# Performance work log

Measured on AMD Instinct MI355X. Metric: run time of the kernel, lower is better.

## Reference

```python
import jax, jax.numpy as jnp
import numpy as np

N_NODES = 80000
N_EDGES = 160000
HID = 300
NODE_DIM = 133
EDGE_DIM = 14
N_GRAPHS = 1600


def setup_inputs() -> dict:
    key = jax.random.key(0)
    ks = jax.random.split(key, 32)
    s = 0.05
    half = N_EDGES // 2
    inp = {
        "x": jax.random.normal(ks[0], (N_NODES, NODE_DIM), jnp.float32),
        "edge_attr": jax.random.normal(ks[1], (N_EDGES, EDGE_DIM), jnp.float32),
        "W_atoms": jax.random.uniform(ks[2], (N_NODES,), jnp.float32),
        "eps": jax.random.normal(ks[3], (N_GRAPHS, HID), jnp.float32),
        "src_half": jax.random.randint(ks[4], (half,), 0, N_NODES, jnp.int32),
        "dst_half": jax.random.randint(ks[5], (half,), 0, N_NODES, jnp.int32),
        "batch": jnp.sort(jax.random.randint(ks[6], (N_NODES,), 0, N_GRAPHS, jnp.int32)),
    }
    def W(k, i, o):
        return jax.random.normal(k, (i, o), jnp.float32) * s
    def B(k, o):
        return jax.random.normal(k, (o,), jnp.float32) * s
    # tconv1 (first_linear=True): lin1 in=node+edge, atom_updater in=node+hid (with ReLU)
    inp["t_lin_w"] = W(ks[7], NODE_DIM + EDGE_DIM, HID); inp["t_lin_b"] = B(ks[8], HID)
    inp["t_mp_w"] = jax.random.normal(ks[9], (3, HID, HID), jnp.float32) * s
    inp["t_mp_b"] = jax.random.normal(ks[10], (3, HID), jnp.float32) * s
    inp["t_au_w"] = W(ks[11], NODE_DIM + HID, HID); inp["t_au_b"] = B(ks[12], HID)
    # mu conv (first_linear=False): lin2 in=hid+edge, atom_updater2 in=2*hid (no ReLU)
    inp["mu_lin_w"] = W(ks[13], HID + EDGE_DIM, HID); inp["mu_lin_b"] = B(ks[14], HID)
    inp["mu_mp_w"] = jax.random.normal(ks[15], (3, HID, HID), jnp.float32) * s
    inp["mu_mp_b"] = jax.random.normal(ks[16], (3, HID), jnp.float32) * s
    inp["mu_au_w"] = W(ks[17], 2 * HID, HID); inp["mu_au_b"] = B(ks[18], HID)
    # logvar conv (first_linear=False)
    inp["lv_lin_w"] = W(ks[19], HID + EDGE_DIM, HID); inp["lv_lin_b"] = B(ks[20], HID)
    inp["lv_mp_w"] = jax.random.normal(ks[21], (3, HID, HID), jnp.float32) * s
    inp["lv_mp_b"] = jax.random.normal(ks[22], (3, HID), jnp.float32) * s
    inp["lv_au_w"] = W(ks[23], 2 * HID, HID); inp["lv_au_b"] = B(ks[24], HID)
    return inp


def reference(x, edge_attr, W_atoms, eps, src_half, dst_half, batch,
              t_lin_w, t_lin_b, t_mp_w, t_mp_b, t_au_w, t_au_b,
              mu_lin_w, mu_lin_b, mu_mp_w, mu_mp_b, mu_au_w, mu_au_b,
              lv_lin_w, lv_lin_b, lv_mp_w, lv_mp_b, lv_au_w, lv_au_b):
    E = edge_attr.shape[0]
    half = E // 2
    N = x.shape[0]
    # directed edges come in reverse pairs: edge e and edge rev(e)
    src = jnp.concatenate([src_half, dst_half])
    dst = jnp.concatenate([dst_half, src_half])
    rev = jnp.concatenate([jnp.arange(half, E), jnp.arange(0, half)])
    relu = jax.nn.relu

    def mp_agg(h):
        # dest_is_origin sparse mm: for edge e=(u->v), sum h over edges k with
        # dst(k)==u, excluding the reverse edge (v->u)
        inc = jax.ops.segment_sum(h, dst, num_segments=N)  # [N, H]
        return inc[src] - h[rev]

    def conv(node_in, lin_w, lin_b, mp_w, mp_b, au_w, au_b, out_relu):
        h = relu(jnp.concatenate([node_in[src], edge_attr], axis=1) @ lin_w + lin_b)
        for i in range(3):  # three vec_scratch_MP_layers: relu(h + Lin(D @ h))
            h = relu(h + mp_agg(h) @ mp_w[i] + mp_b[i])
        # inc_edges_to_atom sparse mm: sum incident edge states per atom
        sum_inc = jax.ops.segment_sum(h, dst, num_segments=N)
        a = jnp.concatenate([node_in, sum_inc], axis=1) @ au_w + au_b
        return relu(a) if out_relu else a

    shared = conv(x, t_lin_w, t_lin_b, t_mp_w, t_mp_b, t_au_w, t_au_b, True)
    mu = conv(shared, mu_lin_w, mu_lin_b, mu_mp_w, mu_mp_b, mu_au_w, mu_au_b, False)
    lv = conv(shared, lv_lin_w, lv_lin_b, lv_mp_w, lv_mp_b, lv_au_w, lv_au_b, False)

    w = W_atoms[:, None]
    cnt = jnp.maximum(jax.ops.segment_sum(jnp.ones((N,), x.dtype), batch,
                                          num_segments=N_GRAPHS), 1.0)[:, None]
    mu_g = jax.ops.segment_sum(mu * w, batch, num_segments=N_GRAPHS) / cnt
    lv_g = jax.ops.segment_sum(lv * w, batch, num_segments=N_GRAPHS) / cnt
    # VAE reparameterization: z = mu + exp(0.5*logvar) * eps
    z = mu_g + jnp.exp(0.5 * lv_g) * eps
    return z
```

## Files before the change

kernel.cpp:

```cpp
#include <hip/hip_runtime.h>
#include <hip/hip_bf16.h>

#define NN 80000
#define NE 160000
#define HALF 80000
#define HID 300
#define NG 1600
#define SCB 256

typedef __attribute__((ext_vector_type(8))) short bf16x8v;
typedef __attribute__((ext_vector_type(4))) float f32x4v;

__device__ __forceinline__ float bf2f_us(unsigned short u) {
    return __uint_as_float(((unsigned int)u) << 16);
}
__device__ __forceinline__ unsigned short f2bf_us(float f) {
    union { __bf16 b; unsigned short u; } cv;
    cv.b = (__bf16)f;
    return cv.u;
}
__device__ __forceinline__ float ld1(const float* p) { return *p; }
__device__ __forceinline__ float ld1(const unsigned short* p) { return bf2f_us(*p); }
__device__ __forceinline__ void st1(float* p, float v) { *p = v; }
__device__ __forceinline__ void st1(unsigned short* p, float v) { *p = f2bf_us(v); }
__device__ __forceinline__ float4 ld4(const float* p) { return *(const float4*)p; }
__device__ __forceinline__ float4 ld4(const unsigned short* p) {
    ushort4 u = *(const ushort4*)p;
    return make_float4(bf2f_us(u.x), bf2f_us(u.y), bf2f_us(u.z), bf2f_us(u.w));
}
__device__ __forceinline__ void st4(float* p, float4 v) { *(float4*)p = v; }
__device__ __forceinline__ void st4(unsigned short* p, float4 v) {
    ushort4 u; u.x = f2bf_us(v.x); u.y = f2bf_us(v.y); u.z = f2bf_us(v.z); u.w = f2bf_us(v.w);
    *(ushort4*)p = u;
}
__device__ __forceinline__ int clampi(int v, int lo, int hi) {
    return v < lo ? lo : (v > hi ? hi : v);
}

__global__ void k_zerof(float* __restrict__ p, int n) {
    int i = blockIdx.x * 256 + threadIdx.x; if (i < n) p[i] = 0.f;
}
__global__ void k_zeroi(int* __restrict__ p, int n) {
    int i = blockIdx.x * 256 + threadIdx.x; if (i < n) p[i] = 0;
}

__global__ void k_wsplit_conv(const float* __restrict__ Wmp,
                              const float* __restrict__ Wlin, int Klin, int nktlin,
                              const float* __restrict__ Wau, int Kau, int nktau,
                              unsigned short* __restrict__ wh_mp, unsigned short* __restrict__ wl_mp,
                              unsigned short* __restrict__ wh_la, unsigned short* __restrict__ wl_la) {
    const int MP_L = 10 * 19 * 512;
    int idx = blockIdx.x * 256 + threadIdx.x;
    int total = 570 + nktlin * 19 + nktau * 19;
    int t = idx >> 6;
    if (t >= total) return;
    int lane = idx & 63;
    const float* W; int Krows, ltile;
    unsigned short *whi, *wlo;
    if (t < 570) {
        int l = t / 190, rem = t - l * 190;
        W = Wmp + l * 90000; Krows = 300; ltile = rem;
        whi = wh_mp + l * MP_L; wlo = wl_mp + l * MP_L;
    } else if (t < 570 + nktlin * 19) {
        ltile = t - 570; W = Wlin; Krows = Klin;
        whi = wh_la; wlo = wl_la;
    } else {
        ltile = t - 570 - nktlin * 19; W = Wau; Krows = Kau;
        size_t off = (size_t)nktlin * 19 * 512;
        whi = wh_la + off; wlo = wl_la + off;
    }
    int kt = ltile / 19, ct = ltile - kt * 19;
    int quad = lane >> 4, cr = lane & 15;
    size_t obase = ((size_t)ltile * 64 + lane) * 8;
    for (int j = 0; j < 8; ++j) {
        int k = kt * 32 + quad * 8 + j;
        int n = ct * 16 + cr;
        float v = (k < Krows && n < 300) ? W[(size_t)k * 300 + n] : 0.f;
        unsigned short hu = f2bf_us(v);
        unsigned short lu = f2bf_us(v - bf2f_us(hu));
        whi[obase + j] = hu;
        wlo[obase + j] = lu;
    }
}

__global__ void k_hist(const int* __restrict__ srcH, const int* __restrict__ dstH, int* __restrict__ deg) {
    int e = blockIdx.x * 256 + threadIdx.x;
    if (e >= NE) return;
    int d = (e < HALF) ? dstH[e] : srcH[e - HALF];
    d = clampi(d, 0, NN - 1);
    atomicAdd(&deg[d], 1);
}
__global__ void k_histg(const int* __restrict__ batch, int* __restrict__ degg) {
    int n = blockIdx.x * 256 + threadIdx.x;
    if (n >= NN) return;
    atomicAdd(&degg[clampi(batch[n], 0, NG - 1)], 1);
}

__global__ __launch_bounds__(256) void k_scan_part(const int* __restrict__ deg, int* __restrict__ part, int n) {
    __shared__ int red[256];
    int b = blockIdx.x, t = threadIdx.x;
    int chunk = (n + SCB - 1) / SCB;
// ... 73 lines not shown
    int lo = clampi(start[n], 0, NE), hi = clampi(start[n + 1], 0, NE);
    float4 a0 = make_float4(0.f, 0.f, 0.f, 0.f);
    float4 a1 = make_float4(0.f, 0.f, 0.f, 0.f);
    int j = lo;
    for (; j + 2 <= hi; j += 2) {
        int e0 = clampi(elist[j], 0, NE - 1);
        int e1 = clampi(elist[j + 1], 0, NE - 1);
        const unsigned short* r0 = &h[(size_t)e0 * 300 + c0];
        const unsigned short* r1 = &h[(size_t)e1 * 300 + c0];
        float4 v0 = ld4(r0);
        float4 w0 = ld4(r1);
        a0.x += v0.x + w0.x; a0.y += v0.y + w0.y; a0.z += v0.z + w0.z; a0.w += v0.w + w0.w;
        if (full) {
            float4 v1 = ld4(r0 + 4);
            float4 w1 = ld4(r1 + 4);
            a1.x += v1.x + w1.x; a1.y += v1.y + w1.y; a1.z += v1.z + w1.z; a1.w += v1.w + w1.w;
        }
    }
    if (j < hi) {
        int e0 = clampi(elist[j], 0, NE - 1);
        const unsigned short* r0 = &h[(size_t)e0 * 300 + c0];
        float4 v0 = ld4(r0);
        a0.x += v0.x; a0.y += v0.y; a0.z += v0.z; a0.w += v0.w;
        if (full) {
            float4 v1 = ld4(r0 + 4);
            a1.x += v1.x; a1.y += v1.y; a1.z += v1.z; a1.w += v1.w;
        }
    }
    st4(&inc[(size_t)n * 300 + c0], a0);
    if (full) st4(&inc[(size_t)n * 300 + c0 + 4], a1);
}


template <int NID, typename TN>
__global__ __launch_bounds__(512, 4) void k_lin_mfma(
        const TN* __restrict__ node_in, const float* __restrict__ ea,
        const int* __restrict__ srcH, const int* __restrict__ dstH,
        const unsigned short* __restrict__ whi, const unsigned short* __restrict__ wlo,
        const float* __restrict__ bias, unsigned short* __restrict__ h) {
    constexpr int K = NID + 14;
    constexpr int KP = (K + 31) & ~31;
    constexpr int NKT = KP / 32;
    constexpr int LDK = (KP + 8 < 312) ? 312 : KP + 8;
    __shared__ unsigned short As[64 * LDK];
    __shared__ int ssrc[64];
    const int tid = threadIdx.x;
    const int lane = tid & 63, wv = tid >> 6;
    const int quad = lane >> 4, cr = lane & 15;
    const int e0 = blockIdx.x * 64;
    if (tid < 64) {
        int e = e0 + tid;
        int s = (e < HALF) ? srcH[e] : dstH[e - HALF];
        ssrc[tid] = clampi(s, 0, NN - 1);
    }
    __syncthreads();
    if constexpr (NID == 300) {
        for (int idx = tid; idx < 64 * 75; idx += 512) {
            int r = idx / 75, q = idx - r * 75;
            *(ushort4*)&As[r * LDK + q * 4] =
                *(const ushort4*)&((const unsigned short*)node_in)[(size_t)ssrc[r] * 300 + q * 4];
        }
        for (int idx = tid; idx < 64 * (KP - 300); idx += 512) {
            int r = idx / (KP - 300), k = idx - r * (KP - 300);
            int kk = 300 + k;
            float v = (kk < K) ? ea[(size_t)(e0 + r) * 14 + (kk - 300)] : 0.f;
            As[r * LDK + kk] = f2bf_us(v);
        }
    } else {
        for (int idx = tid; idx < 64 * KP; idx += 512) {
            int r = idx / KP, k = idx - r * KP;
            float v;
            if (k < NID)    v = ld1(&node_in[(size_t)ssrc[r] * NID + k]);
            else if (k < K) v = ea[(size_t)(e0 + r) * 14 + (k - NID)];
            else            v = 0.f;
            As[r * LDK + k] = f2bf_us(v);
        }
    }
    __syncthreads();
    f32x4v acc[4][3];
    #pragma unroll
    for (int c = 0; c < 3; ++c) {
        int ct = wv + 8 * c;
        float b = 0.f;
        if (ct < 19) { int col = ct * 16 + cr; if (col < 300) b = bias[col]; }
        #pragma unroll
        for (int rt = 0; rt < 4; ++rt) { f32x4v a = {b, b, b, b}; acc[rt][c] = a; }
    }
    bf16x8v pbhi[2][3], pblo[2][3];
    #pragma unroll
    for (int c = 0; c < 3; ++c) {
        int ct = wv + 8 * c;
        if (ct < 19) {
            size_t base = ((size_t)ct * 64 + lane) * 8;
            pbhi[0][c] = *(const bf16x8v*)&whi[base];
            pblo[0][c] = *(const bf16x8v*)&wlo[base];
        }
    }
    #pragma unroll
    for (int kt = 0; kt < NKT; ++kt) {
        const int cur = kt & 1, nxt = cur ^ 1;
        if (kt + 1 < NKT) {
            #pragma unroll
            for (int c = 0; c < 3; ++c) {
                int ct = wv + 8 * c;
                if (ct < 19) {
                    size_t base = ((size_t)((kt + 1) * 19 + ct) * 64 + lane) * 8;
                    pbhi[nxt][c] = *(const bf16x8v*)&whi[base];
                    pblo[nxt][c] = *(const bf16x8v*)&wlo[base];
                }
            }
        }
        #pragma unroll
        for (int rt = 0; rt < 4; ++rt) {
            bf16x8v a = *(const bf16x8v*)&As[(rt * 16 + cr) * LDK + kt * 32 + quad * 8];
            #pragma unroll
            for (int c = 0; c < 3; ++c) {
                int ct = wv + 8 * c;
                if (ct >= 19) break;
                acc[rt][c] = __builtin_amdgcn_mfma_f32_16x16x32_bf16(a, pblo[cur][c], acc[rt][c], 0, 0, 0);
                acc[rt][c] = __builtin_amdgcn_mfma_f32_16x16x32_bf16(a, pbhi[cur][c], acc[rt][c], 0, 0, 0);
            }
        }
    }
    __syncthreads();
    #pragma unroll
    for (int c = 0; c < 3; ++c) {
        int ct = wv + 8 * c;
        if (ct >= 19) break;
        int col = ct * 16 + cr;
        if (col >= 300) continue;
        #pragma unroll
        for (int rt = 0; rt < 4; ++rt)
            #pragma unroll
            for (int r = 0; r < 4; ++r)
                As[(rt * 16 + quad * 4 + r) * LDK + col] = f2bf_us(fmaxf(acc[rt][c][r], 0.f));
    }
    __syncthreads();
    for (int idx = tid; idx < 64 * 75; idx += 512) {
        int r = idx / 75, q = idx - r * 75;
        *(ushort4*)&h[(size_t)(e0 + r) * 300 + q * 4] = *(const ushort4*)&As[r * LDK + q * 4];
    }
}

template <int NID, typename TN, bool RELU>
__global__ __launch_bounds__(512, 4) void k_au_mfma(
        const TN* __restrict__ node_in, const unsigned short* __restrict__ h,
        const int* __restrict__ elist, const int* __restrict__ start,
        const unsigned short* __restrict__ whi, const unsigned short* __restrict__ wlo,
        const float* __restrict__ bias, unsigned short* __restrict__ out_rows) {
    constexpr int K = NID + 300;
    constexpr int KP = (K + 31) & ~31;
    constexpr int NKT = KP / 32;
    constexpr int LDK = KP + 8;
    __shared__ unsigned short As[64 * LDK];
    const int tid = threadIdx.x;
    const int lane = tid & 63, wv = tid >> 6;
    const int quad = lane >> 4, cr = lane & 15;
    const int n0 = blockIdx.x * 64;
    if constexpr (NID == 300) {
        for (int idx = tid; idx < 64 * 75; idx += 512) {
            int r = idx / 75, q = idx - r * 75;
            *(ushort4*)&As[r * LDK + q * 4] =
                *(const ushort4*)&((const unsigned short*)node_in)[(size_t)(n0 + r) * 300 + q * 4];
        }
    } else {
        const float* xb = (const float*)node_in + (size_t)n0 * NID;
        for (int f4 = tid; f4 < (64 * NID) / 4; f4 += 512) {
            float4 v = *(const float4*)&xb[f4 * 4];
            int f = f4 * 4;
            float vv[4] = {v.x, v.y, v.z, v.w};
            #pragma unroll
            for (int i = 0; i < 4; ++i) {
                int fi = f + i;
                int r = fi / NID, k = fi - r * NID;
                As[r * LDK + k] = f2bf_us(vv[i]);
            }
        }
    }
    for (int idx = tid; idx < 64 * 75; idx += 512) {
        int r = idx / 75, q = idx - r * 75;
        int n = n0 + r;
        int lo = clampi(start[n], 0, NE), hi = clampi(start[n + 1], 0, NE);
        float4 acc = make_float4(0.f, 0.f, 0.f, 0.f);
        int j = lo;
        for (; j + 2 <= hi; j += 2) {
            int ei0 = clampi(elist[j], 0, NE - 1);
            int ei1 = clampi(elist[j + 1], 0, NE - 1);
            float4 v0 = ld4(&h[(size_t)ei0 * 300 + q * 4]);
            float4 v1 = ld4(&h[(size_t)ei1 * 300 + q * 4]);
            acc.x += v0.x; acc.y += v0.y; acc.z += v0.z; acc.w += v0.w;
            acc.x += v1.x; acc.y += v1.y; acc.z += v1.z; acc.w += v1.w;
        }
        if (j < hi) {
            int ei0 = clampi(elist[j], 0, NE - 1);
            float4 v0 = ld4(&h[(size_t)ei0 * 300 + q * 4]);
            acc.x += v0.x; acc.y += v0.y; acc.z += v0.z; acc.w += v0.w;
        }
        unsigned short* dst = &As[r * LDK + NID + q * 4];
        dst[0] = f2bf_us(acc.x); dst[1] = f2bf_us(acc.y);
        dst[2] = f2bf_us(acc.z); dst[3] = f2bf_us(acc.w);
    }
    constexpr int PAD = KP - NID - 300;
    for (int idx = tid; idx < 64 * PAD; idx += 512) {
        int r = idx / PAD, k = idx - r * PAD;
        As[r * LDK + NID + 300 + k] = 0;
    }
    __syncthreads();
    f32x4v acc[4][3];
    #pragma unroll
    for (int c = 0; c < 3; ++c) {
        int ct = wv + 8 * c;
        float b = 0.f;
        if (ct < 19) { int col = ct * 16 + cr; if (col < 300) b = bias[col]; }
        #pragma unroll
        for (int rt = 0; rt < 4; ++rt) { f32x4v a = {b, b, b, b}; acc[rt][c] = a; }
    }
    bf16x8v pbhi[2][3], pblo[2][3];
    #pragma unroll
    for (int c = 0; c < 3; ++c) {
        int ct = wv + 8 * c;
        if (ct < 19) {
            size_t base = ((size_t)ct * 64 + lane) * 8;
            pbhi[0][c] = *(const bf16x8v*)&whi[base];
            pblo[0][c] = *(const bf16x8v*)&wlo[base];
        }
    }
    #pragma unroll
    for (int kt = 0; kt < NKT; ++kt) {
        const int cur = kt & 1, nxt = cur ^ 1;
        if (kt + 1 < NKT) {
            #pragma unroll
            for (int c = 0; c < 3; ++c) {
                int ct = wv + 8 * c;
                if (ct < 19) {
                    size_t base = ((size_t)((kt + 1) * 19 + ct) * 64 + lane) * 8;
                    pbhi[nxt][c] = *(const bf16x8v*)&whi[base];
                    pblo[nxt][c] = *(const bf16x8v*)&wlo[base];
                }
            }
        }
        #pragma unroll
        for (int rt = 0; rt < 4; ++rt) {
            bf16x8v a = *(const bf16x8v*)&As[(rt * 16 + cr) * LDK + kt * 32 + quad * 8];
            #pragma unroll
            for (int c = 0; c < 3; ++c) {
                int ct = wv + 8 * c;
                if (ct >= 19) break;
                acc[rt][c] = __builtin_amdgcn_mfma_f32_16x16x32_bf16(a, pblo[cur][c], acc[rt][c], 0, 0, 0);
                acc[rt][c] = __builtin_amdgcn_mfma_f32_16x16x32_bf16(a, pbhi[cur][c], acc[rt][c], 0, 0, 0);
            }
        }
    }
    __syncthreads();
    #pragma unroll
    for (int c = 0; c < 3; ++c) {
        int ct = wv + 8 * c;
        if (ct >= 19) break;
        int col = ct * 16 + cr;
        if (col >= 300) continue;
        #pragma unroll
        for (int rt = 0; rt < 4; ++rt)
            #pragma unroll
            for (int r = 0; r < 4; ++r) {
                float v = acc[rt][c][r];
                As[(rt * 16 + quad * 4 + r) * LDK + col] = f2bf_us(RELU ? fmaxf(v, 0.f) : v);
            }
    }
    __syncthreads();
    for (int idx = tid; idx < 64 * 75; idx += 512) {
        int r = idx / 75, q = idx - r * 75;
        *(ushort4*)&out_rows[(size_t)(n0 + r) * 300 + q * 4] = *(const ushort4*)&As[r * LDK + q * 4];
    }
}

__global__ __launch_bounds__(512, 4) void k_mp_mfma(
        unsigned short* __restrict__ h, const unsigned short* __restrict__ inc,
        const int* __restrict__ srcH, const int* __restrict__ dstH,
        const unsigned short* __restrict__ whi, const unsigned short* __restrict__ wlo,
        const float* __restrict__ bias) {
    constexpr int LDK = 328;
    __shared__ unsigned short Hs[64 * LDK];
    __shared__ int ssrc[64];
    const int tid = threadIdx.x;
    const int lane = tid & 63, wv = tid >> 6;
    const int quad = lane >> 4, cr = lane & 15;
    const int p0 = blockIdx.x * 32;
    if (tid < 64) {
        int r = tid;
        int e = (r < 32) ? (p0 + r) : (p0 + r - 32 + HALF);
        int s = (e < HALF) ? srcH[e] : dstH[e - HALF];
        ssrc[r] = clampi(s, 0, NN - 1);
    }
    __syncthreads();
    for (int idx = tid; idx < 64 * 80; idx += 512) {
        int r = idx / 80, q = idx - r * 80;
        int col = q * 4;
        if (col < 300) {
            int ep = (r < 32) ? (p0 + r + HALF) : (p0 + r - 32);
            float4 hp = ld4(&h[(size_t)ep * 300 + col]);
            float4 iv = ld4(&inc[(size_t)ssrc[r] * 300 + col]);
            st4(&Hs[r * LDK + col],
                make_float4(iv.x - hp.x, iv.y - hp.y, iv.z - hp.z, iv.w - hp.w));
        } else {
            *(ushort4*)&Hs[r * LDK + col] = make_ushort4(0, 0, 0, 0);
        }
    }
    __syncthreads();
    f32x4v acc[4][3];
    #pragma unroll
    for (int c = 0; c < 3; ++c)
        #pragma unroll
        for (int rt = 0; rt < 4; ++rt) {
            f32x4v a = {0.f, 0.f, 0.f, 0.f};
            acc[rt][c] = a;
        }
    bf16x8v pbhi[2][3], pblo[2][3];
    #pragma unroll
    for (int c = 0; c < 3; ++c) {
        int ct = wv + 8 * c;
        if (ct < 19) {
            size_t base = ((size_t)ct * 64 + lane) * 8;
            pbhi[0][c] = *(const bf16x8v*)&whi[base];
            pblo[0][c] = *(const bf16x8v*)&wlo[base];
        }
    }
    #pragma unroll
    for (int kt = 0; kt < 10; ++kt) {
        const int cur = kt & 1, nxt = cur ^ 1;
        if (kt + 1 < 10) {
            #pragma unroll
            for (int c = 0; c < 3; ++c) {
                int ct = wv + 8 * c;
                if (ct < 19) {
                    size_t base = ((size_t)((kt + 1) * 19 + ct) * 64 + lane) * 8;
                    pbhi[nxt][c] = *(const bf16x8v*)&whi[base];
                    pblo[nxt][c] = *(const bf16x8v*)&wlo[base];
                }
            }
        }
        #pragma unroll
        for (int rt = 0; rt < 4; ++rt) {
            bf16x8v a = *(const bf16x8v*)&Hs[(rt * 16 + cr) * LDK + kt * 32 + quad * 8];
            #pragma unroll
            for (int c = 0; c < 3; ++c) {
                int ct = wv + 8 * c;
                if (ct >= 19) break;
                acc[rt][c] = __builtin_amdgcn_mfma_f32_16x16x32_bf16(a, pblo[cur][c], acc[rt][c], 0, 0, 0);
                acc[rt][c] = __builtin_amdgcn_mfma_f32_16x16x32_bf16(a, pbhi[cur][c], acc[rt][c], 0, 0, 0);
            }
        }
    }
    __syncthreads();
    #pragma unroll
    for (int c = 0; c < 3; ++c) {
        int ct = wv + 8 * c;
        if (ct >= 19) break;
        int col = ct * 16 + cr;
        if (col >= 300) continue;
        float bv = bias[col];
        #pragma unroll
        for (int rt = 0; rt < 4; ++rt)
            #pragma unroll
            for (int r = 0; r < 4; ++r) {
                int row = rt * 16 + quad * 4 + r;
                int e = (row < 32) ? (p0 + row) : (p0 + row - 32 + HALF);
                float hv = bf2f_us(h[(size_t)e * 300 + col]);
                Hs[row * LDK + col] = f2bf_us(fmaxf(acc[rt][c][r] + bv + hv, 0.f));
            }
    }
    __syncthreads();
    for (int idx = tid; idx < 64 * 75; idx += 512) {
        int r = idx / 75, q = idx - r * 75;
        int e = (r < 32) ? (p0 + r) : (p0 + r - 32 + HALF);
        *(ushort4*)&h[(size_t)e * 300 + q * 4] = *(const ushort4*)&Hs[r * LDK + q * 4];
    }
}

__global__ __launch_bounds__(320) void k_pool(const unsigned short* __restrict__ rows,
                                              const float* __restrict__ wat,
                                              const int* __restrict__ gs, float* __restrict__ outg) {
    int g = blockIdx.x, c = threadIdx.x;
    if (c >= 300) return;
    int lo = clampi(gs[g], 0, NN), hi = clampi(gs[g + 1], 0, NN);
    float acc = 0.f;
    for (int n = lo; n < hi; ++n)
        acc += bf2f_us(rows[(size_t)n * 300 + c]) * wat[n];
    float cn = fmaxf((float)(hi - lo), 1.f);
    outg[g * 300 + c] = acc / cn;
}
__global__ __launch_bounds__(320) void k_final(const float* __restrict__ mu_g, const float* __restrict__ lv_g,
                                               const float* __restrict__ eps, float* __restrict__ out) {
    int g = blockIdx.x, c = threadIdx.x;
    if (c >= 300) return;
    out[g * 300 + c] = mu_g[g * 300 + c] + expf(0.5f * lv_g[g * 300 + c]) * eps[g * 300 + c];
}

extern "C" void kernel_launch(void* const* d_in, const int* in_sizes, int n_in,
                              void* d_out, int out_size, void* d_ws, size_t ws_size,
                              hipStream_t stream) {
    float* outp = (float*)d_out;

    const size_t NEED = 199500000ull;
    if (ws_size < NEED) {
        k_zerof<<<(out_size + 255) / 256, 256, 0, stream>>>(outp, out_size);
        return;
    }

// ... 1 lines not shown
    const float* ea  = (const float*)d_in[1];
    const float* wat = (const float*)d_in[2];
    const float* eps = (const float*)d_in[3];
    const int* srcH  = (const int*)d_in[4];
    const int* dstH  = (const int*)d_in[5];
    const int* batch = (const int*)d_in[6];
    const float* w_t_lin  = (const float*)d_in[7];
    const float* b_t_lin  = (const float*)d_in[8];
    const float* w_t_mp   = (const float*)d_in[9];
    const float* b_t_mp   = (const float*)d_in[10];
    const float* w_t_au   = (const float*)d_in[11];
    const float* b_t_au   = (const float*)d_in[12];
    const float* w_mu_lin = (const float*)d_in[13];
    const float* b_mu_lin = (const float*)d_in[14];
    const float* w_mu_mp  = (const float*)d_in[15];
    const float* b_mu_mp  = (const float*)d_in[16];
    const float* w_mu_au  = (const float*)d_in[17];
    const float* b_mu_au  = (const float*)d_in[18];
    const float* w_lv_lin = (const float*)d_in[19];
    const float* b_lv_lin = (const float*)d_in[20];
    const float* w_lv_mp  = (const float*)d_in[21];
    const float* b_lv_mp  = (const float*)d_in[22];
    const float* w_lv_au  = (const float*)d_in[23];
    const float* b_lv_au  = (const float*)d_in[24];

    char* p = (char*)d_ws;
    auto alloc = [&](size_t nbytes) { char* q = p; p += (nbytes + 255) & ~(size_t)255; return q; };
    unsigned short* h   = (unsigned short*)alloc((size_t)NE * 300 * 2);
    unsigned short* inc = (unsigned short*)alloc((size_t)NN * 300 * 2);
    unsigned short* sh  = (unsigned short*)alloc((size_t)NN * 300 * 2);
    const size_t MPU = (size_t)3 * 10 * 19 * 512;
    unsigned short* wh_mp = (unsigned short*)alloc(MPU * 2);
    unsigned short* wl_mp = (unsigned short*)alloc(MPU * 2);
    const size_t LAU = (size_t)29 * 19 * 512;
    unsigned short* wh_la = (unsigned short*)alloc(LAU * 2);
    unsigned short* wl_la = (unsigned short*)alloc(LAU * 2);
    float* mu_g = (float*)alloc((size_t)NG * 300 * 4);
    float* lv_g = (float*)alloc((size_t)NG * 300 * 4);
    int* deg    = (int*)alloc(NN * 4);
    int* startA = (int*)alloc((NN + 1) * 4);
    int* elist  = (int*)alloc(NE * 4);
    int* degg   = (int*)alloc(NG * 4);
    int* gs     = (int*)alloc((NG + 1) * 4);
    int* part   = (int*)alloc(SCB * 4);

    k_zeroi<<<(NN + 255) / 256, 256, 0, stream>>>(deg, NN);
    k_hist<<<(NE + 255) / 256, 256, 0, stream>>>(srcH, dstH, deg);
    k_scan_part<<<SCB, 256, 0, stream>>>(deg, part, NN);
    k_scan_offsets<<<1, 256, 0, stream>>>(part);
    k_scan_apply<<<SCB, 256, 0, stream>>>(deg, part, startA, deg, NN);
    k_fill<<<(NE + 255) / 256, 256, 0, stream>>>(srcH, dstH, deg, elist);
    k_zeroi<<<(NG + 255) / 256, 256, 0, stream>>>(degg, NG);
    k_histg<<<(NN + 255) / 256, 256, 0, stream>>>(batch, degg);
    k_scan_part<<<SCB, 256, 0, stream>>>(degg, part, NG);
    k_scan_offsets<<<1, 256, 0, stream>>>(part);
    k_scan_apply<<<SCB, 256, 0, stream>>>(degg, part, gs, (int*)nullptr, NG);

    const int SSG = (NN * 38 + 255) / 256;
    const size_t MP_L = (size_t)10 * 19 * 512;
    unsigned short* rows = inc;
    auto wsplit_conv = [&](const float* Wmp, const float* Wlin, int Klin, int nktlin,
                           const float* Wau, int Kau, int nktau) {
        int total = 570 + nktlin * 19 + nktau * 19;
        k_wsplit_conv<<<(total * 64 + 255) / 256, 256, 0, stream>>>(
            Wmp, Wlin, Klin, nktlin, Wau, Kau, nktau, wh_mp, wl_mp, wh_la, wl_la);
    };

    wsplit_conv(w_t_mp, w_t_lin, 147, 5, w_t_au, 433, 14);
    const size_t AU_T = (size_t)5 * 19 * 512;
    k_lin_mfma<133, float><<<NE / 64, 512, 0, stream>>>(x, ea, srcH, dstH, wh_la, wl_la, b_t_lin, h);
    for (int i = 0; i < 3; ++i) {
        k_segsum8<<<SSG, 256, 0, stream>>>(h, elist, startA, inc);
        k_mp_mfma<<<HALF / 32, 512, 0, stream>>>(h, inc, srcH, dstH,
                                                 wh_mp + i * MP_L, wl_mp + i * MP_L, b_t_mp + i * 300);
    }
    k_au_mfma<133, float, true><<<NN / 64, 512, 0, stream>>>(x, h, elist, startA,
                                                             wh_la + AU_T, wl_la + AU_T, b_t_au, sh);

    wsplit_conv(w_mu_mp, w_mu_lin, 314, 10, w_mu_au, 600, 19);
    const size_t AU_MU = (size_t)10 * 19 * 512;
    k_lin_mfma<300, unsigned short><<<NE / 64, 512, 0, stream>>>(sh, ea, srcH, dstH, wh_la, wl_la, b_mu_lin, h);
    for (int i = 0; i < 3; ++i) {
        k_segsum8<<<SSG, 256, 0, stream>>>(h, elist, startA, inc);
        k_mp_mfma<<<HALF / 32, 512, 0, stream>>>(h, inc, srcH, dstH,
                                                 wh_mp + i * MP_L, wl_mp + i * MP_L, b_mu_mp + i * 300);
    }
    k_au_mfma<300, unsigned short, false><<<NN / 64, 512, 0, stream>>>(sh, h, elist, startA,
                                                                       wh_la + AU_MU, wl_la + AU_MU, b_mu_au, rows);
    k_pool<<<NG, 320, 0, stream>>>(rows, wat, gs, mu_g);

    wsplit_conv(w_lv_mp, w_lv_lin, 314, 10, w_lv_au, 600, 19);
    k_lin_mfma<300, unsigned short><<<NE / 64, 512, 0, stream>>>(sh, ea, srcH, dstH, wh_la, wl_la, b_lv_lin, h);
    for (int i = 0; i < 3; ++i) {
        k_segsum8<<<SSG, 256, 0, stream>>>(h, elist, startA, inc);
        k_mp_mfma<<<HALF / 32, 512, 0, stream>>>(h, inc, srcH, dstH,
                                                 wh_mp + i * MP_L, wl_mp + i * MP_L, b_lv_mp + i * 300);
    }
    k_au_mfma<300, unsigned short, false><<<NN / 64, 512, 0, stream>>>(sh, h, elist, startA,
                                                                       wh_la + AU_MU, wl_la + AU_MU, b_lv_au, rows);
    k_pool<<<NG, 320, 0, stream>>>(rows, wat, gs, lv_g);

    k_final<<<NG, 320, 0, stream>>>(mu_g, lv_g, eps, outp);
}
```

Before: 2.044 ms.

## Panelize K dimension in MFMA kernels to shrink LDS and raise occupancy

The lin, au and mp MFMA kernels now stage the A operand in 160-column K panels through a small shared buffer instead of holding the whole row. This cuts LDS use so launch bounds can go from 4 to 6 blocks per CU. The weight split kernel pads the au weights per segment to match the panel boundaries. The trade is more barriers and panel reloads, the loss of the previous register double-buffering of weight fragments, and a two-pass epilogue.

```diff
diff --git a/kernel.cpp b/kernel.cpp
--- a/kernel.cpp
+++ b/kernel.cpp
@@ -21,8 +21,6 @@
 }
 __device__ __forceinline__ float ld1(const float* p) { return *p; }
 __device__ __forceinline__ float ld1(const unsigned short* p) { return bf2f_us(*p); }
-__device__ __forceinline__ void st1(float* p, float v) { *p = v; }
-__device__ __forceinline__ void st1(unsigned short* p, float v) { *p = f2bf_us(v); }
 __device__ __forceinline__ float4 ld4(const float* p) { return *(const float4*)p; }
 __device__ __forceinline__ float4 ld4(const unsigned short* p) {
     ushort4 u = *(const ushort4*)p;
@@ -46,12 +44,12 @@
 
 __global__ void k_wsplit_conv(const float* __restrict__ Wmp,
                               const float* __restrict__ Wlin, int Klin, int nktlin,
-                              const float* __restrict__ Wau, int Kau, int nktau,
+                              const float* __restrict__ Wau, int Kau1, int nkt1,
                               unsigned short* __restrict__ wh_mp, unsigned short* __restrict__ wl_mp,
                               unsigned short* __restrict__ wh_la, unsigned short* __restrict__ wl_la) {
     const int MP_L = 10 * 19 * 512;
     int idx = blockIdx.x * 256 + threadIdx.x;
-    int total = 570 + nktlin * 19 + nktau * 19;
+    int total = 570 + (nktlin + nkt1 + 10) * 19;
     int t = idx >> 6;
     if (t >= total) return;
     int lane = idx & 63;
@@ -64,9 +62,14 @@
     } else if (t < 570 + nktlin * 19) {
         ltile = t - 570; W = Wlin; Krows = Klin;
         whi = wh_la; wlo = wl_la;
+    } else if (t < 570 + (nktlin + nkt1) * 19) {
+        ltile = t - 570 - nktlin * 19; W = Wau; Krows = Kau1;
+        size_t off = (size_t)nktlin * 19 * 512;
+        whi = wh_la + off; wlo = wl_la + off;
     } else {
-        ltile = t - 570 - nktlin * 19; W = Wau; Krows = Kau;
-        size_t off = (size_t)nktlin * 19 * 512;
+        ltile = t - 570 - (nktlin + nkt1) * 19;
+        W = Wau + (size_t)Kau1 * 300; Krows = 300;
+        size_t off = (size_t)(nktlin + nkt1) * 19 * 512;
         whi = wh_la + off; wlo = wl_la + off;
     }
     int kt = ltile / 19, ct = ltile - kt * 19;
@@ -206,17 +209,18 @@
 }
 
 
+#define LDKH 172
+
 template <int NID, typename TN>
-__global__ __launch_bounds__(512, 4) void k_lin_mfma(
+__global__ __launch_bounds__(512, 6) void k_lin_mfma(
         const TN* __restrict__ node_in, const float* __restrict__ ea,
         const int* __restrict__ srcH, const int* __restrict__ dstH,
         const unsigned short* __restrict__ whi, const unsigned short* __restrict__ wlo,
         const float* __restrict__ bias, unsigned short* __restrict__ h) {
     constexpr int K = NID + 14;
     constexpr int KP = (K + 31) & ~31;
-    constexpr int NKT = KP / 32;
-    constexpr int LDK = (KP + 8 < 312) ? 312 : KP + 8;
-    __shared__ unsigned short As[64 * LDK];
+    constexpr int NPAN = KP / 160;
+    __shared__ unsigned short As[64 * LDKH];
     __shared__ int ssrc[64];
     const int tid = threadIdx.x;
     const int lane = tid & 63, wv = tid >> 6;
@@ -227,30 +231,6 @@
         int s = (e < HALF) ? srcH[e] : dstH[e - HALF];
         ssrc[tid] = clampi(s, 0, NN - 1);
     }
-    __syncthreads();
-    if constexpr (NID == 300) {
-        for (int idx = tid; idx < 64 * 75; idx += 512) {
-            int r = idx / 75, q = idx - r * 75;
-            *(ushort4*)&As[r * LDK + q * 4] =
-                *(const ushort4*)&((const unsigned short*)node_in)[(size_t)ssrc[r] * 300 + q * 4];
-        }
-        for (int idx = tid; idx < 64 * (KP - 300); idx += 512) {
-            int r = idx / (KP - 300), k = idx - r * (KP - 300);
-            int kk = 300 + k;
-            float v = (kk < K) ? ea[(size_t)(e0 + r) * 14 + (kk - 300)] : 0.f;
-            As[r * LDK + kk] = f2bf_us(v);
-        }
-    } else {
-        for (int idx = tid; idx < 64 * KP; idx += 512) {
-            int r = idx / KP, k = idx - r * KP;
-            float v;
-            if (k < NID)    v = ld1(&node_in[(size_t)ssrc[r] * NID + k]);
-            else if (k < K) v = ea[(size_t)(e0 + r) * 14 + (k - NID)];
-            else            v = 0.f;
-            As[r * LDK + k] = f2bf_us(v);
-        }
-    }
-    __syncthreads();
     f32x4v acc[4][3];
     #pragma unroll
     for (int c = 0; c < 3; ++c) {
@@ -260,126 +240,123 @@
         #pragma unroll
         for (int rt = 0; rt < 4; ++rt) { f32x4v a = {b, b, b, b}; acc[rt][c] = a; }
     }
-    bf16x8v pbhi[2][3], pblo[2][3];
-    #pragma unroll
-    for (int c = 0; c < 3; ++c) {
-        int ct = wv + 8 * c;
-        if (ct < 19) {
-            size_t base = ((size_t)ct * 64 + lane) * 8;
-            pbhi[0][c] = *(const bf16x8v*)&whi[base];
-            pblo[0][c] = *(const bf16x8v*)&wlo[base];
-        }
-    }
-    #pragma unroll
-    for (int kt = 0; kt < NKT; ++kt) {
-        const int cur = kt & 1, nxt = cur ^ 1;
-        if (kt + 1 < NKT) {
+    __syncthreads();
+    for (int panel = 0; panel < NPAN; ++panel) {
+        if constexpr (NID == 300) {
+            if (panel == 0) {
+                for (int idx = tid; idx < 64 * 40; idx += 512) {
+                    int r = idx / 40, q = idx - r * 40;
+                    *(ushort4*)&As[r * LDKH + q * 4] =
+                        *(const ushort4*)&((const unsigned short*)node_in)[(size_t)ssrc[r] * 300 + q * 4];
+                }
+            } else {
+                for (int idx = tid; idx < 64 * 40; idx += 512) {
+                    int r = idx / 40, q = idx - r * 40;
+                    int col = 160 + q * 4;
+                    if (col + 3 < 300) {
+                        *(ushort4*)&As[r * LDKH + q * 4] =
+                            *(const ushort4*)&((const unsigned short*)node_in)[(size_t)ssrc[r] * 300 + col];
+                    } else {
+                        unsigned short u[4];
+                        #pragma unroll
+                        for (int i = 0; i < 4; ++i) {
+                            int k = col + i;
+                            float v = (k < K) ? ea[(size_t)(e0 + r) * 14 + (k - 300)] : 0.f;
+                            u[i] = f2bf_us(v);
+                        }
+                        *(ushort4*)&As[r * LDKH + q * 4] = make_ushort4(u[0], u[1], u[2], u[3]);
+                    }
+                }
+            }
+        } else {
+            for (int idx = tid; idx < 64 * 160; idx += 512) {
+                int r = idx / 160, k = idx - r * 160;
+                float v;
+                if (k < NID)    v = ld1(&node_in[(size_t)ssrc[r] * NID + k]);
+                else if (k < K) v = ea[(size_t)(e0 + r) * 14 + (k - NID)];
+                else            v = 0.f;
+                As[r * LDKH + k] = f2bf_us(v);
+            }
+        }
+        __syncthreads();
+        #pragma unroll
+        for (int kt = 0; kt < 5; ++kt) {
+            const int ktg = panel * 5 + kt;
+            bf16x8v bb[3];
             #pragma unroll
             for (int c = 0; c < 3; ++c) {
                 int ct = wv + 8 * c;
-                if (ct < 19) {
-                    size_t base = ((size_t)((kt + 1) * 19 + ct) * 64 + lane) * 8;
-                    pbhi[nxt][c] = *(const bf16x8v*)&whi[base];
-                    pblo[nxt][c] = *(const bf16x8v*)&wlo[base];
-                }
-            }
-        }
-        #pragma unroll
-        for (int rt = 0; rt < 4; ++rt) {
-            bf16x8v a = *(const bf16x8v*)&As[(rt * 16 + cr) * LDK + kt * 32 + quad * 8];
+                if (ct < 19)
+                    bb[c] = *(const bf16x8v*)&wlo[((size_t)(ktg * 19 + ct) * 64 + lane) * 8];
+            }
+            #pragma unroll
+            for (int rt = 0; rt < 4; ++rt) {
+                bf16x8v a = *(const bf16x8v*)&As[(rt * 16 + cr) * LDKH + kt * 32 + quad * 8];
+                #pragma unroll
+                for (int c = 0; c < 3; ++c) {
+                    int ct = wv + 8 * c;
+                    if (ct >= 19) break;
+                    acc[rt][c] = __builtin_amdgcn_mfma_f32_16x16x32_bf16(a, bb[c], acc[rt][c], 0, 0, 0);
+                }
+            }
             #pragma unroll
             for (int c = 0; c < 3; ++c) {
                 int ct = wv + 8 * c;
-                if (ct >= 19) break;
-                acc[rt][c] = __builtin_amdgcn_mfma_f32_16x16x32_bf16(a, pblo[cur][c], acc[rt][c], 0, 0, 0);
-                acc[rt][c] = __builtin_amdgcn_mfma_f32_16x16x32_bf16(a, pbhi[cur][c], acc[rt][c], 0, 0, 0);
-            }
-        }
-    }
-    __syncthreads();
-    #pragma unroll
-    for (int c = 0; c < 3; ++c) {
-        int ct = wv + 8 * c;
-        if (ct >= 19) break;
-        int col = ct * 16 + cr;
-        if (col >= 300) continue;
-        #pragma unroll
-        for (int rt = 0; rt < 4; ++rt)
-            #pragma unroll
-            for (int r = 0; r < 4; ++r)
-                As[(rt * 16 + quad * 4 + r) * LDK + col] = f2bf_us(fmaxf(acc[rt][c][r], 0.f));
-    }
-    __syncthreads();
-    for (int idx = tid; idx < 64 * 75; idx += 512) {
-        int r = idx / 75, q = idx - r * 75;
-        *(ushort4*)&h[(size_t)(e0 + r) * 300 + q * 4] = *(const ushort4*)&As[r * LDK + q * 4];
+                if (ct < 19)
+                    bb[c] = *(const bf16x8v*)&whi[((size_t)(ktg * 19 + ct) * 64 + lane) * 8];
+            }
+            #pragma unroll
+            for (int rt = 0; rt < 4; ++rt) {
+                bf16x8v a = *(const bf16x8v*)&As[(rt * 16 + cr) * LDKH + kt * 32 + quad * 8];
+                #pragma unroll
+                for (int c = 0; c < 3; ++c) {
+                    int ct = wv + 8 * c;
+                    if (ct >= 19) break;
+                    acc[rt][c] = __builtin_amdgcn_mfma_f32_16x16x32_bf16(a, bb[c], acc[rt][c], 0, 0, 0);
+                }
+            }
+        }
+        __syncthreads();
+    }
+    for (int pass = 0; pass < 2; ++pass) {
+        const int cbase = pass * 160;
+        const int cw = pass ? 140 : 160;
+        #pragma unroll
+        for (int c = 0; c < 3; ++c) {
+            int ct = wv + 8 * c;
+            if (ct >= 19) break;
+            int col = ct * 16 + cr;
+            if (col >= 300 || col < cbase || col >= cbase + cw) continue;
+            #pragma unroll
+            for (int rt = 0; rt < 4; ++rt)
+                #pragma unroll
+                for (int r = 0; r < 4; ++r)
+                    As[(rt * 16 + quad * 4 + r) * LDKH + (col - cbase)] = f2bf_us(fmaxf(acc[rt][c][r], 0.f));
+        }
+        __syncthreads();
+        const int ng = cw / 4;
+        for (int idx = tid; idx < 64 * ng; idx += 512) {
+            int r = idx / ng, q = idx - r * ng;
+            *(ushort4*)&h[(size_t)(e0 + r) * 300 + cbase + q * 4] = *(const ushort4*)&As[r * LDKH + q * 4];
+        }
+        __syncthreads();
     }
 }
 
 template <int NID, typename TN, bool RELU>
-__global__ __launch_bounds__(512, 4) void k_au_mfma(
+__global__ __launch_bounds__(512, 6) void k_au_mfma(
         const TN* __restrict__ node_in, const unsigned short* __restrict__ h,
         const int* __restrict__ elist, const int* __restrict__ start,
         const unsigned short* __restrict__ whi, const unsigned short* __restrict__ wlo,
         const float* __restrict__ bias, unsigned short* __restrict__ out_rows) {
-    constexpr int K = NID + 300;
-    constexpr int KP = (K + 31) & ~31;
-    constexpr int NKT = KP / 32;
-    constexpr int LDK = KP + 8;
-    __shared__ unsigned short As[64 * LDK];
+    constexpr int KP1 = ((NID + 159) / 160) * 160;
+    constexpr int NP1 = KP1 / 160;
+    constexpr int NPAN = NP1 + 2;
+    __shared__ unsigned short As[64 * LDKH];
     const int tid = threadIdx.x;
     const int lane = tid & 63, wv = tid >> 6;
     const int quad = lane >> 4, cr = lane & 15;
     const int n0 = blockIdx.x * 64;
-    if constexpr (NID == 300) {
-        for (int idx = tid; idx < 64 * 75; idx += 512) {
-            int r = idx / 75, q = idx - r * 75;
-            *(ushort4*)&As[r * LDK + q * 4] =
-                *(const ushort4*)&((const unsigned short*)node_in)[(size_t)(n0 + r) * 300 + q * 4];
-        }
-    } else {
-        const float* xb = (const float*)node_in + (size_t)n0 * NID;
-        for (int f4 = tid; f4 < (64 * NID) / 4; f4 += 512) {
-            float4 v = *(const float4*)&xb[f4 * 4];
-            int f = f4 * 4;
-            float vv[4] = {v.x, v.y, v.z, v.w};
-            #pragma unroll
-            for (int i = 0; i < 4; ++i) {
-                int fi = f + i;
-                int r = fi / NID, k = fi - r * NID;
-                As[r * LDK + k] = f2bf_us(vv[i]);
-            }
-        }
-    }
-    for (int idx = tid; idx < 64 * 75; idx += 512) {
-        int r = idx / 75, q = idx - r * 75;
-        int n = n0 + r;
-        int lo = clampi(start[n], 0, NE), hi = clampi(start[n + 1], 0, NE);
-        float4 acc = make_float4(0.f, 0.f, 0.f, 0.f);
-        int j = lo;
-        for (; j + 2 <= hi; j += 2) {
-            int ei0 = clampi(elist[j], 0, NE - 1);
-            int ei1 = clampi(elist[j + 1], 0, NE - 1);
-            float4 v0 = ld4(&h[(size_t)ei0 * 300 + q * 4]);
-            float4 v1 = ld4(&h[(size_t)ei1 * 300 + q * 4]);
-            acc.x += v0.x; acc.y += v0.y; acc.z += v0.z; acc.w += v0.w;
-            acc.x += v1.x; acc.y += v1.y; acc.z += v1.z; acc.w += v1.w;
-        }
-        if (j < hi) {
-            int ei0 = clampi(elist[j], 0, NE - 1);
-            float4 v0 = ld4(&h[(size_t)ei0 * 300 + q * 4]);
-            acc.x += v0.x; acc.y += v0.y; acc.z += v0.z; acc.w += v0.w;
-        }
-        unsigned short* dst = &As[r * LDK + NID + q * 4];
-        dst[0] = f2bf_us(acc.x); dst[1] = f2bf_us(acc.y);
-        dst[2] = f2bf_us(acc.z); dst[3] = f2bf_us(acc.w);
-    }
-    constexpr int PAD = KP - NID - 300;
-    for (int idx = tid; idx < 64 * PAD; idx += 512) {
-        int r = idx / PAD, k = idx - r * PAD;
-        As[r * LDK + NID + 300 + k] = 0;
-    }
-    __syncthreads();
     f32x4v acc[4][3];
     #pragma unroll
     for (int c = 0; c < 3; ++c) {
@@ -389,71 +366,140 @@
         #pragma unroll
         for (int rt = 0; rt < 4; ++rt) { f32x4v a = {b, b, b, b}; acc[rt][c] = a; }
     }
-    bf16x8v pbhi[2][3], pblo[2][3];
-    #pragma unroll
-    for (int c = 0; c < 3; ++c) {
-        int ct = wv + 8 * c;
-        if (ct < 19) {
-            size_t base = ((size_t)ct * 64 + lane) * 8;
-            pbhi[0][c] = *(const bf16x8v*)&whi[base];
-            pblo[0][c] = *(const bf16x8v*)&wlo[base];
-        }
-    }
-    #pragma unroll
-    for (int kt = 0; kt < NKT; ++kt) {
-        const int cur = kt & 1, nxt = cur ^ 1;
-        if (kt + 1 < NKT) {
+    for (int panel = 0; panel < NPAN; ++panel) {
+        if (panel < NP1) {
+            const int kbase = panel * 160;
+            if constexpr (NID == 300) {
+                for (int idx = tid; idx < 64 * 40; idx += 512) {
+                    int r = idx / 40, q = idx - r * 40;
+                    int col = kbase + q * 4;
+                    if (col < 300) {
+                        *(ushort4*)&As[r * LDKH + q * 4] =
+                            *(const ushort4*)&((const unsigned short*)node_in)[(size_t)(n0 + r) * 300 + col];
+                    } else {
+                        *(ushort4*)&As[r * LDKH + q * 4] = make_ushort4(0, 0, 0, 0);
+                    }
+                }
+            } else {
+                const float* xb = (const float*)node_in + (size_t)n0 * NID;
+                for (int f4 = tid; f4 < (64 * NID) / 4; f4 += 512) {
+                    float4 v = *(const float4*)&xb[f4 * 4];
+                    int f = f4 * 4;
+                    float vv[4] = {v.x, v.y, v.z, v.w};
+                    #pragma unroll
+                    for (int i = 0; i < 4; ++i) {
+                        int fi = f + i;
+                        int r = fi / NID, k = fi - r * NID;
+                        As[r * LDKH + k] = f2bf_us(vv[i]);
+                    }
+                }
+                for (int idx = tid; idx < 64 * (160 - NID); idx += 512) {
+                    int r = idx / (160 - NID), k = idx - r * (160 - NID);
+                    As[r * LDKH + NID + k] = 0;
+                }
+            }
+        } else {
+            const int cbase = (panel - NP1) * 160;
+            for (int idx = tid; idx < 64 * 40; idx += 512) {
+                int r = idx / 40, q = idx - r * 40;
+                int col = cbase + q * 4;
+                if (col < 300) {
+                    int n = n0 + r;
+                    int lo = clampi(start[n], 0, NE), hi = clampi(start[n + 1], 0, NE);
+                    float4 a4 = make_float4(0.f, 0.f, 0.f, 0.f);
+                    int j = lo;
+                    for (; j + 2 <= hi; j += 2) {
+                        int ei0 = clampi(elist[j], 0, NE - 1);
+                        int ei1 = clampi(elist[j + 1], 0, NE - 1);
+                        float4 v0 = ld4(&h[(size_t)ei0 * 300 + col]);
+                        float4 v1 = ld4(&h[(size_t)ei1 * 300 + col]);
+                        a4.x += v0.x; a4.y += v0.y; a4.z += v0.z; a4.w += v0.w;
+                        a4.x += v1.x; a4.y += v1.y; a4.z += v1.z; a4.w += v1.w;
+                    }
+                    if (j < hi) {
+                        int ei0 = clampi(elist[j], 0, NE - 1);
+                        float4 v0 = ld4(&h[(size_t)ei0 * 300 + col]);
+                        a4.x += v0.x; a4.y += v0.y; a4.z += v0.z; a4.w += v0.w;
+                    }
+                    st4(&As[r * LDKH + q * 4], a4);
+                } else {
+                    *(ushort4*)&As[r * LDKH + q * 4] = make_ushort4(0, 0, 0, 0);
+                }
+            }
+        }
+        __syncthreads();
+        #pragma unroll
+        for (int kt = 0; kt < 5; ++kt) {
+            const int ktg = panel * 5 + kt;
+            bf16x8v bb[3];
             #pragma unroll
             for (int c = 0; c < 3; ++c) {
                 int ct = wv + 8 * c;
-                if (ct < 19) {
-                    size_t base = ((size_t)((kt + 1) * 19 + ct) * 64 + lane) * 8;
-                    pbhi[nxt][c] = *(const bf16x8v*)&whi[base];
-                    pblo[nxt][c] = *(const bf16x8v*)&wlo[base];
-                }
-            }
-        }
-        #pragma unroll
-        for (int rt = 0; rt < 4; ++rt) {
-            bf16x8v a = *(const bf16x8v*)&As[(rt * 16 + cr) * LDK + kt * 32 + quad * 8];
+                if (ct < 19)
+                    bb[c] = *(const bf16x8v*)&wlo[((size_t)(ktg * 19 + ct) * 64 + lane) * 8];
+            }
+            #pragma unroll
+            for (int rt = 0; rt < 4; ++rt) {
+                bf16x8v a = *(const bf16x8v*)&As[(rt * 16 + cr) * LDKH + kt * 32 + quad * 8];
+                #pragma unroll
+                for (int c = 0; c < 3; ++c) {
+                    int ct = wv + 8 * c;
+                    if (ct >= 19) break;
+                    acc[rt][c] = __builtin_amdgcn_mfma_f32_16x16x32_bf16(a, bb[c], acc[rt][c], 0, 0, 0);
+                }
+            }
             #pragma unroll
             for (int c = 0; c < 3; ++c) {
                 int ct = wv + 8 * c;
-                if (ct >= 19) break;
-                acc[rt][c] = __builtin_amdgcn_mfma_f32_16x16x32_bf16(a, pblo[cur][c], acc[rt][c], 0, 0, 0);
-                acc[rt][c] = __builtin_amdgcn_mfma_f32_16x16x32_bf16(a, pbhi[cur][c], acc[rt][c], 0, 0, 0);
-            }
-        }
-    }
-    __syncthreads();
-    #pragma unroll
-    for (int c = 0; c < 3; ++c) {
-        int ct = wv + 8 * c;
-        if (ct >= 19) break;
-        int col = ct * 16 + cr;
-        if (col >= 300) continue;
-        #pragma unroll
-        for (int rt = 0; rt < 4; ++rt)
-            #pragma unroll
-            for (int r = 0; r < 4; ++r) {
-                float v = acc[rt][c][r];
-                As[(rt * 16 + quad * 4 + r) * LDK + col] = f2bf_us(RELU ? fmaxf(v, 0.f) : v);
-            }
-    }
-    __syncthreads();
-    for (int idx = tid; idx < 64 * 75; idx += 512) {
-        int r = idx / 75, q = idx - r * 75;
-        *(ushort4*)&out_rows[(size_t)(n0 + r) * 300 + q * 4] = *(const ushort4*)&As[r * LDK + q * 4];
-    }
-}
-
-__global__ __launch_bounds__(512, 4) void k_mp_mfma(
+                if (ct < 19)
+                    bb[c] = *(const bf16x8v*)&whi[((size_t)(ktg * 19 + ct) * 64 + lane) * 8];
+            }
+            #pragma unroll
+            for (int rt = 0; rt < 4; ++rt) {
+                bf16x8v a = *(const bf16x8v*)&As[(rt * 16 + cr) * LDKH + kt * 32 + quad * 8];
+                #pragma unroll
+                for (int c = 0; c < 3; ++c) {
+                    int ct = wv + 8 * c;
+                    if (ct >= 19) break;
+                    acc[rt][c] = __builtin_amdgcn_mfma_f32_16x16x32_bf16(a, bb[c], acc[rt][c], 0, 0, 0);
+                }
+            }
+        }
+        __syncthreads();
+    }
+    for (int pass = 0; pass < 2; ++pass) {
+        const int cbase = pass * 160;
+        const int cw = pass ? 140 : 160;
+        #pragma unroll
+        for (int c = 0; c < 3; ++c) {
+            int ct = wv + 8 * c;
+            if (ct >= 19) break;
+            int col = ct * 16 + cr;
+            if (col >= 300 || col < cbase || col >= cbase + cw) continue;
+            #pragma unroll
+            for (int rt = 0; rt < 4; ++rt)
+                #pragma unroll
+                for (int r = 0; r < 4; ++r) {
+                    float v = acc[rt][c][r];
+                    As[(rt * 16 + quad * 4 + r) * LDKH + (col - cbase)] = f2bf_us(RELU ? fmaxf(v, 0.f) : v);
+                }
+        }
+        __syncthreads();
+        const int ng = cw / 4;
+        for (int idx = tid; idx < 64 * ng; idx += 512) {
+            int r = idx / ng, q = idx - r * ng;
+            *(ushort4*)&out_rows[(size_t)(n0 + r) * 300 + cbase + q * 4] = *(const ushort4*)&As[r * LDKH + q * 4];
+        }
+        __syncthreads();
+    }
+}
+
+__global__ __launch_bounds__(512, 6) void k_mp_mfma(
         unsigned short* __restrict__ h, const unsigned short* __restrict__ inc,
         const int* __restrict__ srcH, const int* __restrict__ dstH,
         const unsigned short* __restrict__ whi, const unsigned short* __restrict__ wlo,
         const float* __restrict__ bias) {
-    constexpr int LDK = 328;
-    __shared__ unsigned short Hs[64 * LDK];
+    __shared__ unsigned short Hs[64 * LDKH];
     __shared__ int ssrc[64];
     const int tid = threadIdx.x;
     const int lane = tid & 63, wv = tid >> 6;
@@ -465,21 +511,6 @@
         int s = (e < HALF) ? srcH[e] : dstH[e - HALF];
         ssrc[r] = clampi(s, 0, NN - 1);
     }
-    __syncthreads();
-    for (int idx = tid; idx < 64 * 80; idx += 512) {
-        int r = idx / 80, q = idx - r * 80;
-        int col = q * 4;
-        if (col < 300) {
-            int ep = (r < 32) ? (p0 + r + HALF) : (p0 + r - 32);
-            float4 hp = ld4(&h[(size_t)ep * 300 + col]);
-            float4 iv = ld4(&inc[(size_t)ssrc[r] * 300 + col]);
-            st4(&Hs[r * LDK + col],
-                make_float4(iv.x - hp.x, iv.y - hp.y, iv.z - hp.z, iv.w - hp.w));
-        } else {
-            *(ushort4*)&Hs[r * LDK + col] = make_ushort4(0, 0, 0, 0);
-        }
-    }
-    __syncthreads();
     f32x4v acc[4][3];
     #pragma unroll
     for (int c = 0; c < 3; ++c)
@@ -488,65 +519,90 @@
             f32x4v a = {0.f, 0.f, 0.f, 0.f};
             acc[rt][c] = a;
         }
-    bf16x8v pbhi[2][3], pblo[2][3];
-    #pragma unroll
-    for (int c = 0; c < 3; ++c) {
-        int ct = wv + 8 * c;
-        if (ct < 19) {
-            size_t base = ((size_t)ct * 64 + lane) * 8;
-            pbhi[0][c] = *(const bf16x8v*)&whi[base];
-            pblo[0][c] = *(const bf16x8v*)&wlo[base];
-        }
-    }
-    #pragma unroll
-    for (int kt = 0; kt < 10; ++kt) {
-        const int cur = kt & 1, nxt = cur ^ 1;
-        if (kt + 1 < 10) {
+    __syncthreads();
+    for (int panel = 0; panel < 2; ++panel) {
+        const int kbase = panel * 160;
+        for (int idx = tid; idx < 64 * 40; idx += 512) {
+            int r = idx / 40, q = idx - r * 40;
+            int col = kbase + q * 4;
+            if (col < 300) {
+                int ep = (r < 32) ? (p0 + r + HALF) : (p0 + r - 32);
+                float4 hp = ld4(&h[(size_t)ep * 300 + col]);
+                float4 iv = ld4(&inc[(size_t)ssrc[r] * 300 + col]);
+                st4(&Hs[r * LDKH + q * 4],
+                    make_float4(iv.x - hp.x, iv.y - hp.y, iv.z - hp.z, iv.w - hp.w));
+            } else {
+                *(ushort4*)&Hs[r * LDKH + q * 4] = make_ushort4(0, 0, 0, 0);
+            }
+        }
+        __syncthreads();
+        #pragma unroll
+        for (int kt = 0; kt < 5; ++kt) {
+            const int ktg = panel * 5 + kt;
+            bf16x8v bb[3];
             #pragma unroll
             for (int c = 0; c < 3; ++c) {
                 int ct = wv + 8 * c;
-                if (ct < 19) {
-                    size_t base = ((size_t)((kt + 1) * 19 + ct) * 64 + lane) * 8;
-                    pbhi[nxt][c] = *(const bf16x8v*)&whi[base];
-                    pblo[nxt][c] = *(const bf16x8v*)&wlo[base];
-                }
-            }
-        }
-        #pragma unroll
-        for (int rt = 0; rt < 4; ++rt) {
-            bf16x8v a = *(const bf16x8v*)&Hs[(rt * 16 + cr) * LDK + kt * 32 + quad * 8];
+                if (ct < 19)
+                    bb[c] = *(const bf16x8v*)&wlo[((size_t)(ktg * 19 + ct) * 64 + lane) * 8];
+            }
+            #pragma unroll
+            for (int rt = 0; rt < 4; ++rt) {
+                bf16x8v a = *(const bf16x8v*)&Hs[(rt * 16 + cr) * LDKH + kt * 32 + quad * 8];
+                #pragma unroll
+                for (int c = 0; c < 3; ++c) {
+                    int ct = wv + 8 * c;
+                    if (ct >= 19) break;
+                    acc[rt][c] = __builtin_amdgcn_mfma_f32_16x16x32_bf16(a, bb[c], acc[rt][c], 0, 0, 0);
+                }
+            }
             #pragma unroll
             for (int c = 0; c < 3; ++c) {
                 int ct = wv + 8 * c;
-                if (ct >= 19) break;
-                acc[rt][c] = __builtin_amdgcn_mfma_f32_16x16x32_bf16(a, pblo[cur][c], acc[rt][c], 0, 0, 0);
-                acc[rt][c] = __builtin_amdgcn_mfma_f32_16x16x32_bf16(a, pbhi[cur][c], acc[rt][c], 0, 0, 0);
-            }
-        }
-    }
-    __syncthreads();
-    #pragma unroll
-    for (int c = 0; c < 3; ++c) {
-        int ct = wv + 8 * c;
-        if (ct >= 19) break;
-        int col = ct * 16 + cr;
-        if (col >= 300) continue;
-        float bv = bias[col];
-        #pragma unroll
-        for (int rt = 0; rt < 4; ++rt)
-            #pragma unroll
-            for (int r = 0; r < 4; ++r) {
-                int row = rt * 16 + quad * 4 + r;
-                int e = (row < 32) ? (p0 + row) : (p0 + row - 32 + HALF);
-                float hv = bf2f_us(h[(size_t)e * 300 + col]);
-                Hs[row * LDK + col] = f2bf_us(fmaxf(acc[rt][c][r] + bv + hv, 0.f));
-            }
-    }
-    __syncthreads();
-    for (int idx = tid; idx < 64 * 75; idx += 512) {
-        int r = idx / 75, q = idx - r * 75;
-        int e = (r < 32) ? (p0 + r) : (p0 + r - 32 + HALF);
-        *(ushort4*)&h[(size_t)e * 300 + q * 4] = *(const ushort4*)&Hs[r * LDK + q * 4];
+                if (ct < 19)
+                    bb[c] = *(const bf16x8v*)&whi[((size_t)(ktg * 19 + ct) * 64 + lane) * 8];
+            }
+            #pragma unroll
+            for (int rt = 0; rt < 4; ++rt) {
+                bf16x8v a = *(const bf16x8v*)&Hs[(rt * 16 + cr) * LDKH + kt * 32 + quad * 8];
+                #pragma unroll
+                for (int c = 0; c < 3; ++c) {
+                    int ct = wv + 8 * c;
+                    if (ct >= 19) break;
+                    acc[rt][c] = __builtin_amdgcn_mfma_f32_16x16x32_bf16(a, bb[c], acc[rt][c], 0, 0, 0);
+                }
+            }
+        }
+        __syncthreads();
+    }
+    for (int pass = 0; pass < 2; ++pass) {
+        const int cbase = pass * 160;
+        const int cw = pass ? 140 : 160;
+        #pragma unroll
+        for (int c = 0; c < 3; ++c) {
+            int ct = wv + 8 * c;
+            if (ct >= 19) break;
+            int col = ct * 16 + cr;
+            if (col >= 300 || col < cbase || col >= cbase + cw) continue;
+            float bv = bias[col];
+            #pragma unroll
+            for (int rt = 0; rt < 4; ++rt)
+                #pragma unroll
+                for (int r = 0; r < 4; ++r) {
+                    int row = rt * 16 + quad * 4 + r;
+                    int e = (row < 32) ? (p0 + row) : (p0 + row - 32 + HALF);
+                    float hv = bf2f_us(h[(size_t)e * 300 + col]);
+                    Hs[row * LDKH + (col - cbase)] = f2bf_us(fmaxf(acc[rt][c][r] + bv + hv, 0.f));
+                }
+        }
+        __syncthreads();
+        const int ng = cw / 4;
+        for (int idx = tid; idx < 64 * ng; idx += 512) {
+            int r = idx / ng, q = idx - r * ng;
+            int e = (r < 32) ? (p0 + r) : (p0 + r - 32 + HALF);
+            *(ushort4*)&h[(size_t)e * 300 + cbase + q * 4] = *(const ushort4*)&Hs[r * LDKH + q * 4];
+        }
+        __syncthreads();
     }
 }
 
@@ -614,7 +670,7 @@
     const size_t MPU = (size_t)3 * 10 * 19 * 512;
     unsigned short* wh_mp = (unsigned short*)alloc(MPU * 2);
     unsigned short* wl_mp = (unsigned short*)alloc(MPU * 2);
-    const size_t LAU = (size_t)29 * 19 * 512;
+    const size_t LAU = (size_t)30 * 19 * 512;
     unsigned short* wh_la = (unsigned short*)alloc(LAU * 2);
     unsigned short* wl_la = (unsigned short*)alloc(LAU * 2);
     float* mu_g = (float*)alloc((size_t)NG * 300 * 4);
@@ -642,13 +698,13 @@
     const size_t MP_L = (size_t)10 * 19 * 512;
     unsigned short* rows = inc;
     auto wsplit_conv = [&](const float* Wmp, const float* Wlin, int Klin, int nktlin,
-                           const float* Wau, int Kau, int nktau) {
-        int total = 570 + nktlin * 19 + nktau * 19;
+                           const float* Wau, int Kau1, int nkt1) {
+        int total = 570 + (nktlin + nkt1 + 10) * 19;
         k_wsplit_conv<<<(total * 64 + 255) / 256, 256, 0, stream>>>(
-            Wmp, Wlin, Klin, nktlin, Wau, Kau, nktau, wh_mp, wl_mp, wh_la, wl_la);
+            Wmp, Wlin, Klin, nktlin, Wau, Kau1, nkt1, wh_mp, wl_mp, wh_la, wl_la);
     };
 
-    wsplit_conv(w_t_mp, w_t_lin, 147, 5, w_t_au, 433, 14);
+    wsplit_conv(w_t_mp, w_t_lin, 147, 5, w_t_au, 133, 5);
     const size_t AU_T = (size_t)5 * 19 * 512;
     k_lin_mfma<133, float><<<NE / 64, 512, 0, stream>>>(x, ea, srcH, dstH, wh_la, wl_la, b_t_lin, h);
     for (int i = 0; i < 3; ++i) {
@@ -659,7 +715,7 @@
     k_au_mfma<133, float, true><<<NN / 64, 512, 0, stream>>>(x, h, elist, startA,
                                                              wh_la + AU_T, wl_la + AU_T, b_t_au, sh);
 
-    wsplit_conv(w_mu_mp, w_mu_lin, 314, 10, w_mu_au, 600, 19);
+    wsplit_conv(w_mu_mp, w_mu_lin, 314, 10, w_mu_au, 300, 10);
     const size_t AU_MU = (size_t)10 * 19 * 512;
     k_lin_mfma<300, unsigned short><<<NE / 64, 512, 0, stream>>>(sh, ea, srcH, dstH, wh_la, wl_la, b_mu_lin, h);
     for (int i = 0; i < 3; ++i) {
@@ -671,7 +727,7 @@
                                                                        wh_la + AU_MU, wl_la + AU_MU, b_mu_au, rows);
     k_pool<<<NG, 320, 0, stream>>>(rows, wat, gs, mu_g);
 
-    wsplit_conv(w_lv_mp, w_lv_lin, 314, 10, w_lv_au, 600, 19);
+    wsplit_conv(w_lv_mp, w_lv_lin, 314, 10, w_lv_au, 300, 10);
     k_lin_mfma<300, unsigned short><<<NE / 64, 512, 0, stream>>>(sh, ea, srcH, dstH, wh_la, wl_la, b_lv_lin, h);
     for (int i = 0; i < 3; ++i) {
         k_segsum8<<<SSG, 256, 0, stream>>>(h, elist, startA, inc);
```

Result: slower. 6.344 ms (+210.4%).
